# Kernel tuning notes

Hardware: AMD Instinct MI355X
Metric: run time of the kernel (lower is better)

The kernel has to match this reference:

```python
import jax, jax.numpy as jnp
import numpy as np

N_NODES = 10000
N_EDGES = 640000
N_GRAPHS = 64
IN_FEAT = 128
HID = (128, 128)
NUM_CLASS = 10


def setup_inputs() -> dict:
    key = jax.random.key(0)
    ks = jax.random.split(key, 10)
    x = jax.random.normal(ks[0], (N_NODES, IN_FEAT), dtype=jnp.float32)
    edge_index = jax.random.randint(ks[1], (2, N_EDGES), 0, N_NODES, dtype=jnp.int64)
    batch = jnp.sort(jax.random.randint(ks[2], (N_NODES,), 0, N_GRAPHS, dtype=jnp.int64))
    # GCNConv weights (PyG applies x @ W then propagates, bias added after aggregation)
    s1 = 1.0 / np.sqrt(IN_FEAT)
    s2 = 1.0 / np.sqrt(HID[0])
    s3 = 1.0 / np.sqrt(HID[1])
    W1 = jax.random.uniform(ks[3], (IN_FEAT, HID[0]), jnp.float32, -s1, s1)
    b1 = jnp.zeros((HID[0],), jnp.float32)
    W2 = jax.random.uniform(ks[4], (HID[0], HID[1]), jnp.float32, -s2, s2)
    b2 = jnp.zeros((HID[1],), jnp.float32)
    Wlin = jax.random.uniform(ks[5], (HID[1], NUM_CLASS), jnp.float32, -s3, s3)
    blin = jax.random.uniform(ks[6], (NUM_CLASS,), jnp.float32, -s3, s3)
    return {"x": x, "edge_index": edge_index, "batch": batch,
            "W1": W1, "b1": b1, "W2": W2, "b2": b2, "Wlin": Wlin, "blin": blin}


def _gcn_conv(x, src, dst, W, b):
    # GCNConv with self-loops and symmetric normalization:
    # out[i] = sum_{(j->i) in E} d[j]^{-1/2} d[i]^{-1/2} (x_j W) + d[i]^{-1} (x_i W) + b
    # where d = in-degree (on dst) + 1 for the self-loop.
    h = x @ W                                                      # [N, F]
    ones = jnp.ones(src.shape[0], dtype=h.dtype)
    deg = jax.ops.segment_sum(ones, dst, num_segments=x.shape[0]) + 1.0
    dinv = jax.lax.rsqrt(deg)                                      # [N]
    norm = dinv[src] * dinv[dst]                                   # [E]
    agg = jax.ops.segment_sum(h[src] * norm[:, None], dst, num_segments=x.shape[0])
    agg = agg + h * (dinv * dinv)[:, None]                         # self-loop term
    return agg + b


def _global_mean_pool(x, batch, num_graphs):
    sums = jax.ops.segment_sum(x, batch, num_segments=num_graphs)          # [G, F]
    cnt = jax.ops.segment_sum(jnp.ones(x.shape[0], x.dtype), batch, num_segments=num_graphs)
    return sums / jnp.maximum(cnt, 1.0)[:, None]


def reference(x, edge_index, batch, W1, b1, W2, b2, Wlin, blin):
    src, dst = edge_index[0], edge_index[1]
    h = jax.nn.relu(_gcn_conv(x, src, dst, W1, b1))
    h = jax.nn.relu(_gcn_conv(h, src, dst, W2, b2))
    g = _global_mean_pool(h, batch, N_GRAPHS)      # [G, hid1]
    return g @ Wlin + blin                          # [G, num_class]
```

## Files before the change

### kernel.cpp

```cpp
#include <hip/hip_runtime.h>

#define NN 10000
#define NE 640000
#define NG 64
#define NF 128
#define NC 10
#define TMR 16
#define TKC 32
#define NB 250
#define BSZ 40
#define G1 512
#define ECHUNK 1250
#define CAP 32
#define CCAP 3072
#define NSL 64


__device__ __forceinline__ unsigned short f2bf(float f) {
    unsigned int u = __float_as_uint(f);
    return (unsigned short)((u + 0x7FFF + ((u >> 16) & 1)) >> 16);
}
__device__ __forceinline__ float bf_lo(unsigned int p) {
    return __uint_as_float(p << 16);
}
__device__ __forceinline__ float bf_hi(unsigned int p) {
    return __uint_as_float(p & 0xFFFF0000u);
}

__device__ __forceinline__ int detect64(const int* w, long span) {
    int lane = threadIdx.x & 63;
    long e = (long)lane * (span - 1) / 63;
    return (__ballot(w[2 * e + 1] != 0) == 0ULL) ? 1 : 0;
}

__device__ __forceinline__ int ld_idx(const void* p, long i, int is64) {
    return is64 ? (int)((const long long*)p)[i] : ((const int*)p)[i];
}

__global__ __launch_bounds__(256) void k_prep(const void* __restrict__ ei,
                                              const void* __restrict__ batch,
                                              int* __restrict__ bh,
                                              int* __restrict__ ebuf,
                                              float* __restrict__ outacc,
                                              float* __restrict__ cntinv) {
    int is64 = detect64((const int*)ei, NE);
    __shared__ int hist[256];
    __shared__ int cur[256];
    int tid = threadIdx.x;
    hist[tid] = 0;
    __syncthreads();
    if (blockIdx.x < 8) {
        float* base = outacc + (size_t)blockIdx.x * 8 * NG * NC;
        for (int i = tid; i < 8 * NG * NC; i += 256) base[i] = 0.f;
    }
    if (blockIdx.x == 8 && tid < NG) {
        int isb = detect64((const int*)batch, NN / 2);
        int lo0 = 0, hi0 = NN;
        while (lo0 < hi0) {
            int m = (lo0 + hi0) >> 1;
            if (ld_idx(batch, m, isb) < tid) lo0 = m + 1; else hi0 = m;
        }
        int lo1 = lo0, hi1 = NN;
        while (lo1 < hi1) {
            int m = (lo1 + hi1) >> 1;
            if (ld_idx(batch, m, isb) < tid + 1) lo1 = m + 1; else hi1 = m;
        }
        cntinv[tid] = 1.0f / fmaxf((float)(lo1 - lo0), 1.0f);
    }
    int e0 = blockIdx.x * ECHUNK;
    int dstv[5], srcv[5];
#pragma unroll
    for (int i = 0; i < 5; ++i) {
        int r = tid + i * 256;
        if (r < ECHUNK) {
            long e = (long)e0 + r;
            dstv[i] = ld_idx(ei, (long)NE + e, is64);
            srcv[i] = ld_idx(ei, e, is64);
            atomicAdd(&hist[dstv[i] / BSZ], 1);
        } else {
            dstv[i] = -1; srcv[i] = 0;
        }
    }
    __syncthreads();
    if (tid < NB) {
        bh[tid * G1 + blockIdx.x] = min(hist[tid], CAP);
        cur[tid] = (tid * G1 + blockIdx.x) * CAP;
    }
    __syncthreads();
#pragma unroll
    for (int i = 0; i < 5; ++i) {
        if (tid + i * 256 < ECHUNK) {
            int dst = dstv[i], src = srcv[i];
            int b = dst / BSZ;
            int p = atomicAdd(&cur[b], 1);
            int lim = (b * G1 + blockIdx.x) * CAP + CAP;
            if (p < lim) ebuf[p] = ((dst - b * BSZ) << 14) | src;
        }
    }
}

__global__ __launch_bounds__(256) void k_csr(const int* __restrict__ ebuf,
                                             const int* __restrict__ bh,
                                             int* __restrict__ coff,
                                             int* __restrict__ deg,
                                             float* __restrict__ dinv,
                                             unsigned short* __restrict__ csrc) {
    __shared__ int scnt[G1];
    __shared__ int dcount[BSZ];
    __shared__ int dstart[BSZ];
    __shared__ int cur[BSZ];
    int b = blockIdx.x, tid = threadIdx.x;
    for (int i = tid; i < G1; i += 256) scnt[i] = bh[b * G1 + i];
    if (tid < BSZ) dcount[tid] = 0;
    __syncthreads();
    for (int blk = tid; blk < G1; blk += 256) {
        int c = scnt[blk];
        int base = (b * G1 + blk) * CAP;
        for (int i = 0; i < c; ++i)
            atomicAdd(&dcount[ebuf[base + i] >> 14], 1);
    }
    __syncthreads();
    if (tid == 0) {
        int run = 0;
        for (int i = 0; i < BSZ; ++i) {
            dstart[i] = run; cur[i] = b * CCAP + run; run += dcount[i];
        }
    }
    __syncthreads();
    if (tid < BSZ) {
        coff[b * BSZ + tid] = b * CCAP + dstart[tid];
        deg[b * BSZ + tid] = dcount[tid];
        dinv[b * BSZ + tid] = rsqrtf((float)dcount[tid] + 1.0f);
    }
    __syncthreads();
    for (int blk = tid; blk < G1; blk += 256) {
        int c = scnt[blk];
        int base = (b * G1 + blk) * CAP;
        for (int i = 0; i < c; ++i) {
            int pk = ebuf[base + i];
            int p = atomicAdd(&cur[pk >> 14], 1);
            csrc[p] = (unsigned short)(pk & 16383);
        }
    }
}

__global__ __launch_bounds__(256) void k_gemm(const float* __restrict__ X,
                                              const float* __restrict__ W,
                                              const float* __restrict__ dinv,
                                              unsigned short* __restrict__ Y,
                                              int nrows) {
    __shared__ float sX[TKC * 20];
    __shared__ float sW[32 * 132];
    int tid = threadIdx.x;
    int rg = tid & 7;
    int cg = tid >> 3;
    int m0 = blockIdx.x * TMR;
    float acc[2][4] = {{0.f}};
    for (int kc = 0; kc < NF / TKC; ++kc) {
        int k0 = kc * TKC;
        if (tid < 128) {
            int row = tid >> 3, kq = tid & 7;
            int mm = m0 + row; if (mm > nrows - 1) mm = nrows - 1;
            float4 v = *(const float4*)(X + (size_t)mm * NF + k0 + kq * 4);
            sX[(kq * 4 + 0) * 20 + row] = v.x;
            sX[(kq * 4 + 1) * 20 + row] = v.y;
            sX[(kq * 4 + 2) * 20 + row] = v.z;
            sX[(kq * 4 + 3) * 20 + row] = v.w;
        }
#pragma unroll
        for (int j = 0; j < 4; ++j) {
            int idx = tid + 256 * j;
            int k = idx >> 5, cq = idx & 31;
            float4 v = *(const float4*)(W + (size_t)(k0 + k) * NF + cq * 4);
            *(float4*)(sW + cq * 132 + k * 4) = v;
        }
        __syncthreads();
#pragma unroll 8
        for (int k = 0; k < TKC; ++k) {
            float2 xf = *(const float2*)(sX + k * 20 + rg * 2);
            float4 wf = *(const float4*)(sW + cg * 132 + k * 4);
            acc[0][0] = fmaf(xf.x, wf.x, acc[0][0]);
            acc[0][1] = fmaf(xf.x, wf.y, acc[0][1]);
            acc[0][2] = fmaf(xf.x, wf.z, acc[0][2]);
            acc[0][3] = fmaf(xf.x, wf.w, acc[0][3]);
            acc[1][0] = fmaf(xf.y, wf.x, acc[1][0]);
            acc[1][1] = fmaf(xf.y, wf.y, acc[1][1]);
            acc[1][2] = fmaf(xf.y, wf.z, acc[1][2]);
            acc[1][3] = fmaf(xf.y, wf.w, acc[1][3]);
        }
        __syncthreads();
    }
#pragma unroll
    for (int r = 0; r < 2; ++r) {
        int m = m0 + rg * 2 + r;
        if (m < nrows) {
            float ds = dinv[m];
            ushort4 h;
            h.x = f2bf(acc[r][0] * ds);
            h.y = f2bf(acc[r][1] * ds);
            h.z = f2bf(acc[r][2] * ds);
            h.w = f2bf(acc[r][3] * ds);
            *(ushort4*)(Y + (size_t)m * NF + cg * 4) = h;
        }
    }
}

__device__ __forceinline__ void gacc_node(const unsigned short* __restrict__ G,
                                          const unsigned short* __restrict__ csrc,
                                          int beg, int end, int q, int f, int lane,
                                          float a[8]) {
    int dg = end - beg;
    int nreg = min(dg, 128);
    unsigned int sv = 0;
    if (lane < dg) sv = csrc[beg + lane];
    if (64 + lane < dg) sv |= ((unsigned int)csrc[beg + 64 + lane]) << 16;
    int vi = q;
    int nfull = nreg & ~31;
    for (; vi < nfull; vi += 32) {
        int s[8];
#pragma unroll
        for (int j = 0; j < 8; ++j) {
            int e = vi + 4 * j;
            unsigned int w = (unsigned int)__shfl((int)sv, e & 63, 64);
            s[j] = (int)((w >> ((e >> 6) << 4)) & 0xFFFFu);
        }
        uint4 p[8];
#pragma unroll
        for (int j = 0; j < 8; ++j)
            p[j] = ((const uint4*)(G + (size_t)s[j] * NF))[f];
#pragma unroll
        for (int j = 0; j < 8; ++j) {
            a[0] += bf_lo(p[j].x); a[1] += bf_hi(p[j].x);
            a[2] += bf_lo(p[j].y); a[3] += bf_hi(p[j].y);
            a[4] += bf_lo(p[j].z); a[5] += bf_hi(p[j].z);
            a[6] += bf_lo(p[j].w); a[7] += bf_hi(p[j].w);
        }
    }
    int nfull16 = nreg & ~15;
    for (; vi < nfull16; vi += 16) {
        int s[4];
#pragma unroll
        for (int j = 0; j < 4; ++j) {
            int e = vi + 4 * j;
            unsigned int w = (unsigned int)__shfl((int)sv, e & 63, 64);
            s[j] = (int)((w >> ((e >> 6) << 4)) & 0xFFFFu);
        }
        uint4 p[4];
#pragma unroll
        for (int j = 0; j < 4; ++j)
            p[j] = ((const uint4*)(G + (size_t)s[j] * NF))[f];
#pragma unroll
        for (int j = 0; j < 4; ++j) {
            a[0] += bf_lo(p[j].x); a[1] += bf_hi(p[j].x);
            a[2] += bf_lo(p[j].y); a[3] += bf_hi(p[j].y);
            a[4] += bf_lo(p[j].z); a[5] += bf_hi(p[j].z);
            a[6] += bf_lo(p[j].w); a[7] += bf_hi(p[j].w);
        }
    }
    int npad = (nreg + 3) & ~3;
    for (; vi < npad; vi += 4) {
        int e = min(vi, nreg - 1);
        unsigned int w = (unsigned int)__shfl((int)sv, e & 63, 64);
        int s = (int)((w >> ((e >> 6) << 4)) & 0xFFFFu);
        uint4 p = ((const uint4*)(G + (size_t)s * NF))[f];
        if (vi < nreg) {
            a[0] += bf_lo(p.x); a[1] += bf_hi(p.x);
            a[2] += bf_lo(p.y); a[3] += bf_hi(p.y);
            a[4] += bf_lo(p.z); a[5] += bf_hi(p.z);
            a[6] += bf_lo(p.w); a[7] += bf_hi(p.w);
        }
    }
    for (int e2 = beg + 128 + q; e2 < end; e2 += 4) {
        int s = csrc[e2];
        uint4 p = ((const uint4*)(G + (size_t)s * NF))[f];
        a[0] += bf_lo(p.x); a[1] += bf_hi(p.x);
        a[2] += bf_lo(p.y); a[3] += bf_hi(p.y);
        a[4] += bf_lo(p.z); a[5] += bf_hi(p.z);
        a[6] += bf_lo(p.w); a[7] += bf_hi(p.w);
    }
#pragma unroll
    for (int j = 0; j < 8; ++j) a[j] += __shfl_xor(a[j], 16);
#pragma unroll
    for (int j = 0; j < 8; ++j) a[j] += __shfl_xor(a[j], 32);
}

__global__ __launch_bounds__(256, 4) void k_gather(const unsigned short* __restrict__ G,
                                                   const int* __restrict__ off,
                                                   const int* __restrict__ dg,
                                                   const unsigned short* __restrict__ csrc,
                                                   const float* __restrict__ dinv,
                                                   const float* __restrict__ bias,
                                                   float* __restrict__ OUT) {
    int wid = threadIdx.x >> 6, lane = threadIdx.x & 63;
    int q = lane >> 4, f = lane & 15;
    int n = blockIdx.x * 4 + wid;
    if (n >= NN) return;
    int beg = off[n], end = beg + dg[n];
    float din = dinv[n];
    float a[8] = {0.f, 0.f, 0.f, 0.f, 0.f, 0.f, 0.f, 0.f};
    gacc_node(G, csrc, beg, end, q, f, lane, a);
    if (q == 0) {
        uint4 sp = ((const uint4*)(G + (size_t)n * NF))[f];
        float4 b0 = ((const float4*)bias)[2 * f];
        float4 b1 = ((const float4*)bias)[2 * f + 1];
        float4 o0, o1;
        o0.x = fmaxf(fmaf(din, a[0] + bf_lo(sp.x), b0.x), 0.f);
        o0.y = fmaxf(fmaf(din, a[1] + bf_hi(sp.x), b0.y), 0.f);
        o0.z = fmaxf(fmaf(din, a[2] + bf_lo(sp.y), b0.z), 0.f);
        o0.w = fmaxf(fmaf(din, a[3] + bf_hi(sp.y), b0.w), 0.f);
        o1.x = fmaxf(fmaf(din, a[4] + bf_lo(sp.z), b1.x), 0.f);
        o1.y = fmaxf(fmaf(din, a[5] + bf_hi(sp.z), b1.y), 0.f);
        o1.z = fmaxf(fmaf(din, a[6] + bf_lo(sp.w), b1.z), 0.f);
        o1.w = fmaxf(fmaf(din, a[7] + bf_hi(sp.w), b1.w), 0.f);
        ((float4*)(OUT + (size_t)n * NF))[2 * f] = o0;
        ((float4*)(OUT + (size_t)n * NF))[2 * f + 1] = o1;
    }
}

__global__ __launch_bounds__(256, 4) void k_gatherpool(const unsigned short* __restrict__ G,
                                                       const int* __restrict__ off,
                                                       const int* __restrict__ dg,
                                                       const unsigned short* __restrict__ csrc,
                                                       const float* __restrict__ dinv,
                                                       const float* __restrict__ bias,
                                                       const void* __restrict__ batch,
                                                       const float* __restrict__ Wl,
                                                       const float* __restrict__ cntinv,
                                                       float* __restrict__ outacc) {
    __shared__ float sWl2[8 * NC * 16];
    int tid = threadIdx.x;
    for (int i = tid; i < 8 * NC * 16; i += 256) {
        int j = i / (NC * 16);
        int r = i - j * (NC * 16);
        int c = r >> 4, f0 = r & 15;
        sWl2[i] = Wl[(f0 * 8 + j) * NC + c];
    }
    int isb64 = detect64((const int*)batch, NN / 2);
    int wid = tid >> 6, lane = tid & 63;
    int q = lane >> 4, f = lane & 15;
    int n = blockIdx.x * 4 + wid;
    int beg = off[n], end = beg + dg[n];
    float din = dinv[n];
    float a[8] = {0.f, 0.f, 0.f, 0.f, 0.f, 0.f, 0.f, 0.f};
    __syncthreads();
    gacc_node(G, csrc, beg, end, q, f, lane, a);
    int g = ld_idx(batch, n, isb64);
    uint4 sp = ((const uint4*)(G + (size_t)n * NF))[f];
    float4 b0 = ((const float4*)bias)[2 * f];
    float4 b1 = ((const float4*)bias)[2 * f + 1];
    float h[8];
    h[0] = fmaxf(fmaf(din, a[0] + bf_lo(sp.x), b0.x), 0.f);
    h[1] = fmaxf(fmaf(din, a[1] + bf_hi(sp.x), b0.y), 0.f);
    h[2] = fmaxf(fmaf(din, a[2] + bf_lo(sp.y), b0.z), 0.f);
    h[3] = fmaxf(fmaf(din, a[3] + bf_hi(sp.y), b0.w), 0.f);
    h[4] = fmaxf(fmaf(din, a[4] + bf_lo(sp.z), b1.x), 0.f);
    h[5] = fmaxf(fmaf(din, a[5] + bf_hi(sp.z), b1.y), 0.f);
    h[6] = fmaxf(fmaf(din, a[6] + bf_lo(sp.w), b1.z), 0.f);
    h[7] = fmaxf(fmaf(din, a[7] + bf_hi(sp.w), b1.w), 0.f);
    float p[NC];
#pragma unroll
    for (int c = 0; c < NC; ++c) p[c] = 0.f;
#pragma unroll
    for (int j = 0; j < 8; ++j) {
        const float* wrow = sWl2 + j * (NC * 16) + f;
#pragma unroll
        for (int c = 0; c < NC; ++c) p[c] = fmaf(h[j], wrow[c * 16], p[c]);
    }
#pragma unroll
    for (int c = 0; c < NC; ++c) {
        p[c] += __shfl_xor(p[c], 1);
        p[c] += __shfl_xor(p[c], 2);
        p[c] += __shfl_xor(p[c], 4);
        p[c] += __shfl_xor(p[c], 8);
    }
    if (lane == 0) {
        float ci = cntinv[g];
        float* dst = outacc + (size_t)(blockIdx.x & (NSL - 1)) * NG * NC + g * NC;
#pragma unroll
        for (int c = 0; c < NC; ++c) atomicAdd(dst + c, p[c] * ci);
    }
}

__global__ __launch_bounds__(256) void k_fin(const float* __restrict__ outacc,
                                             const float* __restrict__ bl,
                                             float* __restrict__ out) {
    int tid = threadIdx.x;
    for (int i = tid; i < NG * NC; i += 256) {
        float s = 0.f;
#pragma unroll 8
        for (int sl = 0; sl < NSL; ++sl) s += outacc[(size_t)sl * NG * NC + i];
        out[i] = s + bl[i % NC];
    }
}

extern "C" void kernel_launch(void* const* d_in, const int* in_sizes, int n_in,
                              void* d_out, int out_size, void* d_ws, size_t ws_size,
                              hipStream_t stream) {
    const float* x  = (const float*)d_in[0];
    const void*  ei = d_in[1];
    const void*  bt = d_in[2];
    const float* W1 = (const float*)d_in[3];
    const float* b1 = (const float*)d_in[4];
    const float* W2 = (const float*)d_in[5];
    const float* b2 = (const float*)d_in[6];
    const float* Wl = (const float*)d_in[7];
    const float* bl = (const float*)d_in[8];

    char* ws = (char*)d_ws;
    int*            coff   = (int*)(ws + 0);
    int*            deg    = (int*)(ws + 40000);
    float*          dinv   = (float*)(ws + 80000);
    float*          outacc = (float*)(ws + 120000);
    float*          cntinv = (float*)(ws + 283840);
    unsigned short* csrc   = (unsigned short*)(ws + 284160);
    unsigned short* Gb     = (unsigned short*)(ws + 2201088);
    float*          bufB   = (float*)(ws + 4761088);
    int*            bh     = (int*)(ws + 2201088);
    int*            ebuf   = (int*)(ws + 4761088);

    k_prep<<<G1, 256, 0, stream>>>(ei, bt, bh, ebuf, outacc, cntinv);
    k_csr <<<NB, 256, 0, stream>>>(ebuf, bh, coff, deg, dinv, csrc);

    k_gemm<<<(NN + TMR - 1) / TMR, 256, 0, stream>>>(x, W1, dinv, Gb, NN);
    k_gather<<<(NN + 3) / 4, 256, 0, stream>>>(Gb, coff, deg, csrc, dinv, b1, bufB);
    k_gemm<<<(NN + TMR - 1) / TMR, 256, 0, stream>>>(bufB, W2, dinv, Gb, NN);
    k_gatherpool<<<(NN + 3) / 4, 256, 0, stream>>>(Gb, coff, deg, csrc, dinv, b2,
                                                   bt, Wl, cntinv, outacc);
    k_fin<<<1, 256, 0, stream>>>(outacc, bl, (float*)d_out);
}
```

Measured before the change: 171.9 us.

## Stage CSR bucket edges in LDS with prefix scans; stage gather indices in LDS

k_csr now computes a wave-level prefix scan over per-cell counts, copies each bucket's edges into a contiguous shared-memory buffer, and runs the degree count and scatter as flat loops over that buffer. The serial single-thread prefix over 40 destinations is replaced by a wave shuffle scan. This removes the uneven per-cell inner loops and repeated global ebuf reads. The gather helper now loads up to 192 source indices into a per-wave LDS array instead of packing 128 into registers and extracting them with shuffles, which handles higher-degree nodes without the global fallback loop but adds LDS traffic. The LDS writes and reads within a wave rely on wave-synchronous execution, with no barrier between them.

Result: faster. 165.9 us (-3.4%).

```diff
diff --git a/kernel.cpp b/kernel.cpp
--- a/kernel.cpp
+++ b/kernel.cpp
@@ -14,6 +14,7 @@
 #define CAP 32
 #define CCAP 3072
 #define NSL 64
+#define MAXD 192
 
 
 __device__ __forceinline__ unsigned short f2bf(float f) {
@@ -106,41 +107,66 @@
                                              float* __restrict__ dinv,
                                              unsigned short* __restrict__ csrc) {
     __shared__ int scnt[G1];
+    __shared__ int cbase[G1];
+    __shared__ int wsum[4];
+    __shared__ int eb[CCAP];
     __shared__ int dcount[BSZ];
-    __shared__ int dstart[BSZ];
     __shared__ int cur[BSZ];
     int b = blockIdx.x, tid = threadIdx.x;
+    int lane = tid & 63, wv = tid >> 6;
     for (int i = tid; i < G1; i += 256) scnt[i] = bh[b * G1 + i];
     if (tid < BSZ) dcount[tid] = 0;
     __syncthreads();
-    for (int blk = tid; blk < G1; blk += 256) {
-        int c = scnt[blk];
-        int base = (b * G1 + blk) * CAP;
-        for (int i = 0; i < c; ++i)
-            atomicAdd(&dcount[ebuf[base + i] >> 14], 1);
-    }
-    __syncthreads();
-    if (tid == 0) {
-        int run = 0;
-        for (int i = 0; i < BSZ; ++i) {
-            dstart[i] = run; cur[i] = b * CCAP + run; run += dcount[i];
-        }
-    }
-    __syncthreads();
-    if (tid < BSZ) {
-        coff[b * BSZ + tid] = b * CCAP + dstart[tid];
-        deg[b * BSZ + tid] = dcount[tid];
-        dinv[b * BSZ + tid] = rsqrtf((float)dcount[tid] + 1.0f);
-    }
-    __syncthreads();
-    for (int blk = tid; blk < G1; blk += 256) {
-        int c = scnt[blk];
-        int base = (b * G1 + blk) * CAP;
-        for (int i = 0; i < c; ++i) {
-            int pk = ebuf[base + i];
-            int p = atomicAdd(&cur[pk >> 14], 1);
-            csrc[p] = (unsigned short)(pk & 16383);
-        }
+    int v0 = scnt[2 * tid], v1 = scnt[2 * tid + 1];
+    int lsum = v0 + v1;
+    int pref = lsum;
+    for (int o = 1; o < 64; o <<= 1) {
+        int t = __shfl_up(pref, o, 64);
+        if (lane >= o) pref += t;
+    }
+    if (lane == 63) wsum[wv] = pref;
+    __syncthreads();
+    int off = 0;
+#pragma unroll
+    for (int j = 0; j < 4; ++j) if (j < wv) off += wsum[j];
+    int ex = pref - lsum + off;
+    cbase[2 * tid] = ex;
+    cbase[2 * tid + 1] = ex + v0;
+    int tot = wsum[0] + wsum[1] + wsum[2] + wsum[3];
+    if (tot > CCAP) tot = CCAP;
+    __syncthreads();
+#pragma unroll
+    for (int cp = 0; cp < 2; ++cp) {
+        int cell = 2 * tid + cp;
+        int c = scnt[cell], lb = cbase[cell];
+        int gb = (b * G1 + cell) * CAP;
+        if (lb + c > CCAP) c = max(0, CCAP - lb);
+        for (int i = 0; i < c; ++i) eb[lb + i] = ebuf[gb + i];
+    }
+    __syncthreads();
+    for (int i = tid; i < tot; i += 256)
+        atomicAdd(&dcount[eb[i] >> 14], 1);
+    __syncthreads();
+    if (tid < 64) {
+        int d = (tid < BSZ) ? dcount[tid] : 0;
+        int pr = d;
+        for (int o = 1; o < 64; o <<= 1) {
+            int t = __shfl_up(pr, o, 64);
+            if (tid >= o) pr += t;
+        }
+        if (tid < BSZ) {
+            int st = pr - d;
+            cur[tid] = b * CCAP + st;
+            coff[b * BSZ + tid] = b * CCAP + st;
+            deg[b * BSZ + tid] = d;
+            dinv[b * BSZ + tid] = rsqrtf((float)d + 1.0f);
+        }
+    }
+    __syncthreads();
+    for (int i = tid; i < tot; i += 256) {
+        int pk = eb[i];
+        int p = atomicAdd(&cur[pk >> 14], 1);
+        csrc[p] = (unsigned short)(pk & 16383);
     }
 }
 
@@ -207,23 +233,18 @@
 
 __device__ __forceinline__ void gacc_node(const unsigned short* __restrict__ G,
                                           const unsigned short* __restrict__ csrc,
+                                          unsigned short* ls,
                                           int beg, int end, int q, int f, int lane,
                                           float a[8]) {
     int dg = end - beg;
-    int nreg = min(dg, 128);
-    unsigned int sv = 0;
-    if (lane < dg) sv = csrc[beg + lane];
-    if (64 + lane < dg) sv |= ((unsigned int)csrc[beg + 64 + lane]) << 16;
+    int nst = min(dg, MAXD);
+    for (int i = lane; i < nst; i += 64) ls[i] = csrc[beg + i];
     int vi = q;
-    int nfull = nreg & ~31;
+    int nfull = nst & ~31;
     for (; vi < nfull; vi += 32) {
         int s[8];
 #pragma unroll
-        for (int j = 0; j < 8; ++j) {
-            int e = vi + 4 * j;
-            unsigned int w = (unsigned int)__shfl((int)sv, e & 63, 64);
-            s[j] = (int)((w >> ((e >> 6) << 4)) & 0xFFFFu);
-        }
+        for (int j = 0; j < 8; ++j) s[j] = ls[vi + 4 * j];
         uint4 p[8];
 #pragma unroll
         for (int j = 0; j < 8; ++j)
@@ -236,15 +257,11 @@
             a[6] += bf_lo(p[j].w); a[7] += bf_hi(p[j].w);
         }
     }
-    int nfull16 = nreg & ~15;
+    int nfull16 = nst & ~15;
     for (; vi < nfull16; vi += 16) {
         int s[4];
 #pragma unroll
-        for (int j = 0; j < 4; ++j) {
-            int e = vi + 4 * j;
-            unsigned int w = (unsigned int)__shfl((int)sv, e & 63, 64);
-            s[j] = (int)((w >> ((e >> 6) << 4)) & 0xFFFFu);
-        }
+        for (int j = 0; j < 4; ++j) s[j] = ls[vi + 4 * j];
         uint4 p[4];
 #pragma unroll
         for (int j = 0; j < 4; ++j)
@@ -257,20 +274,18 @@
             a[6] += bf_lo(p[j].w); a[7] += bf_hi(p[j].w);
         }
     }
-    int npad = (nreg + 3) & ~3;
+    int npad = (nst + 3) & ~3;
     for (; vi < npad; vi += 4) {
-        int e = min(vi, nreg - 1);
-        unsigned int w = (unsigned int)__shfl((int)sv, e & 63, 64);
-        int s = (int)((w >> ((e >> 6) << 4)) & 0xFFFFu);
+        int s = ls[min(vi, nst - 1)];
         uint4 p = ((const uint4*)(G + (size_t)s * NF))[f];
-        if (vi < nreg) {
+        if (vi < nst) {
             a[0] += bf_lo(p.x); a[1] += bf_hi(p.x);
             a[2] += bf_lo(p.y); a[3] += bf_hi(p.y);
             a[4] += bf_lo(p.z); a[5] += bf_hi(p.z);
             a[6] += bf_lo(p.w); a[7] += bf_hi(p.w);
         }
     }
-    for (int e2 = beg + 128 + q; e2 < end; e2 += 4) {
+    for (int e2 = beg + MAXD + q; e2 < end; e2 += 4) {
         int s = csrc[e2];
         uint4 p = ((const uint4*)(G + (size_t)s * NF))[f];
         a[0] += bf_lo(p.x); a[1] += bf_hi(p.x);
@@ -291,6 +306,7 @@
                                                    const float* __restrict__ dinv,
                                                    const float* __restrict__ bias,
                                                    float* __restrict__ OUT) {
+    __shared__ unsigned short lsbuf[4][MAXD];
     int wid = threadIdx.x >> 6, lane = threadIdx.x & 63;
     int q = lane >> 4, f = lane & 15;
     int n = blockIdx.x * 4 + wid;
@@ -298,7 +314,7 @@
     int beg = off[n], end = beg + dg[n];
     float din = dinv[n];
     float a[8] = {0.f, 0.f, 0.f, 0.f, 0.f, 0.f, 0.f, 0.f};
-    gacc_node(G, csrc, beg, end, q, f, lane, a);
+    gacc_node(G, csrc, lsbuf[wid], beg, end, q, f, lane, a);
     if (q == 0) {
         uint4 sp = ((const uint4*)(G + (size_t)n * NF))[f];
         float4 b0 = ((const float4*)bias)[2 * f];
@@ -328,6 +344,7 @@
                                                        const float* __restrict__ cntinv,
                                                        float* __restrict__ outacc) {
     __shared__ float sWl2[8 * NC * 16];
+    __shared__ unsigned short lsbuf[4][MAXD];
     int tid = threadIdx.x;
     for (int i = tid; i < 8 * NC * 16; i += 256) {
         int j = i / (NC * 16);
@@ -343,7 +360,7 @@
     float din = dinv[n];
     float a[8] = {0.f, 0.f, 0.f, 0.f, 0.f, 0.f, 0.f, 0.f};
     __syncthreads();
-    gacc_node(G, csrc, beg, end, q, f, lane, a);
+    gacc_node(G, csrc, lsbuf[wid], beg, end, q, f, lane, a);
     int g = ld_idx(batch, n, isb64);
     uint4 sp = ((const uint4*)(G + (size_t)n * NF))[f];
     float4 b0 = ((const float4*)bias)[2 * f];
```
